# Kernel tuning notes

Measured on AMD Instinct MI355X. Metric: run time of the kernel, lower is better.

## Reference

```python
import jax, jax.numpy as jnp
import numpy as np

H = 16          # nhead
N_LAYERS = 4    # stacks (weights are SHARED across stacks, as in the torch module)
PAD_IDX = 1
EPS = 1e-6
NEG = -1e9


def _pos_encoding(S, d):
    den = jnp.exp(-jnp.arange(0, d, 2, dtype=jnp.float32) * (np.log(10000.0) / d))
    ang = jnp.arange(S, dtype=jnp.float32)[:, None] * den[None, :]  # (S, d/2)
    pe = jnp.zeros((S, d), jnp.float32)
    pe = pe.at[:, 0::2].set(jnp.sin(ang)).at[:, 1::2].set(jnp.cos(ang))
    return pe


def _layer_norm(x, g, b):
    mu = jnp.mean(x, axis=-1, keepdims=True)
    var = jnp.mean((x - mu) ** 2, axis=-1, keepdims=True)
    return (x - mu) * jax.lax.rsqrt(var + EPS) * g + b


def _split_heads(x):
    B, S, d = x.shape
    return x.reshape(B, S, H, d // H).transpose(0, 2, 1, 3)  # (B,H,S,dk)


def _mha(q_in, k_in, v_in, mask, wq, bq, wk, bk, wv, bv, wo, bo):
    q = _split_heads(q_in @ wq + bq)
    k = _split_heads(k_in @ wk + bk)
    v = _split_heads(v_in @ wv + bv)
    dk = v.shape[-1]
    score = jnp.einsum('bhqd,bhkd->bhqk', q, k) / jnp.sqrt(jnp.float32(dk))
    if mask is not None:
        score = jnp.where(mask, score, NEG)
    p = jax.nn.softmax(score, axis=-1)
    out = jnp.einsum('bhqk,bhkd->bhqd', p, v)
    B, _, S, _ = out.shape
    out = out.transpose(0, 2, 1, 3).reshape(B, S, H * dk)
    return out @ wo + bo


def setup_inputs() -> dict:
    key = jax.random.key(0)
    B, St, Sm, d, dff, V = 4, 1024, 1024, 1024, 4096, 32000
    ks = jax.random.split(key, 32)
    sc = 1.0 / np.sqrt(d)
    inp = {
        'target_result': jax.random.randint(ks[0], (B, St), 0, V),
        'memory': jax.random.normal(ks[1], (B, Sm, d), jnp.float32),
        'emb': jax.random.normal(ks[2], (V, d), jnp.float32) * sc,
        'ff_w1': jax.random.normal(ks[3], (d, dff), jnp.float32) * sc,
        'ff_b1': jnp.zeros((dff,), jnp.float32),
        'ff_w2': jax.random.normal(ks[4], (dff, d), jnp.float32) / np.sqrt(dff),
        'ff_b2': jnp.zeros((d,), jnp.float32),
        'ln_g': jnp.ones((d,), jnp.float32),
        'ln_b': jnp.zeros((d,), jnp.float32),
    }
    i = 5
    for pre in ('sa', 'xa'):
        for nm in ('q', 'k', 'v', 'o'):
            inp[f'{pre}_w{nm}'] = jax.random.normal(ks[i], (d, d), jnp.float32) * sc
            inp[f'{pre}_b{nm}'] = jnp.zeros((d,), jnp.float32)
            i += 1
    return inp


def reference(target_result, memory, emb,
              sa_wq, sa_bq, sa_wk, sa_bk, sa_wv, sa_bv, sa_wo, sa_bo,
              xa_wq, xa_bq, xa_wk, xa_bk, xa_wv, xa_bv, xa_wo, xa_bo,
              ff_w1, ff_b1, ff_w2, ff_b2, ln_g, ln_b):
    B, St = target_result.shape
    d = emb.shape[1]
    # embed + scale + positional encoding (dropout = eval/identity)
    x = emb[target_result] * jnp.sqrt(jnp.float32(d)) + _pos_encoding(St, d)[None]
    # masks: pad mask (B,1,St,1) & causal (St,St) -> (B,1,St,St); source mask all-ones -> None
    pad = (target_result != PAD_IDX)[:, None, :, None]
    causal = jnp.tril(jnp.ones((St, St), bool))[None, None]
    tgt_mask = pad & causal
    out = x
    for _ in range(N_LAYERS):
        n = _layer_norm(out, ln_g, ln_b)
        out = out + _mha(n, n, n, tgt_mask,
                         sa_wq, sa_bq, sa_wk, sa_bk, sa_wv, sa_bv, sa_wo, sa_bo)
        n = _layer_norm(out, ln_g, ln_b)
        out = out + _mha(n, memory, memory, None,
                         xa_wq, xa_bq, xa_wk, xa_bk, xa_wv, xa_bv, xa_wo, xa_bo)
        n = _layer_norm(out, ln_g, ln_b)
        out = out + (jax.nn.relu(n @ ff_w1 + ff_b1) @ ff_w2 + ff_b2)
    return _layer_norm(out, ln_g, ln_b)
```

## Files before the change

kernel.cpp:

```cpp
#include <hip/hip_runtime.h>

typedef unsigned short u16;
typedef unsigned int u32;
typedef float f32x4 __attribute__((ext_vector_type(4)));
typedef float f32x16 __attribute__((ext_vector_type(16)));
typedef __bf16 bf16x8 __attribute__((ext_vector_type(8)));
typedef short short8 __attribute__((ext_vector_type(8)));
typedef u32 u32x4 __attribute__((ext_vector_type(4)));

#define DINLINE static __device__ __forceinline__

DINLINE u16 f2bf(float f) {
  u32 u = __builtin_bit_cast(u32, f);
  u += 0x7fffu + ((u >> 16) & 1u);
  return (u16)(u >> 16);
}

DINLINE f32x4 mfma16(short8 a, short8 b, f32x4 c) {
  return __builtin_amdgcn_mfma_f32_16x16x32_bf16(
      __builtin_bit_cast(bf16x8, a), __builtin_bit_cast(bf16x8, b), c, 0, 0, 0);
}

DINLINE f32x16 mfma32(short8 a, short8 b, f32x16 c) {
  return __builtin_amdgcn_mfma_f32_32x32x16_bf16(
      __builtin_bit_cast(bf16x8, a), __builtin_bit_cast(bf16x8, b), c, 0, 0, 0);
}

DINLINE u32 cvtpk(float lo, float hi) {
  u32 r;
  asm("v_cvt_pk_bf16_f32 %0, %1, %2" : "=v"(r) : "v"(lo), "v"(hi));
  return r;
}

DINLINE void plswap(u32& a, u32& b) {
  auto r = __builtin_amdgcn_permlane32_swap(a, b, false, false);
  a = (u32)r[0];
  b = (u32)r[1];
}

DINLINE void gld16(const void* g, void* l) {
  __builtin_amdgcn_global_load_lds(
      (const __attribute__((address_space(1))) void*)g,
      (__attribute__((address_space(3))) void*)l, 16, 0, 0);
}

__global__ __launch_bounds__(256) void transpose_wt(const float* __restrict__ src,
                                                    u16* __restrict__ dst, int K, int N,
                                                    float scale) {
  __shared__ float tile[32][33];
  int n0 = blockIdx.x * 32, k0 = blockIdx.y * 32;
  int tx = threadIdx.x, ty = threadIdx.y;
#pragma unroll
  for (int j = 0; j < 32; j += 8)
    tile[ty + j][tx] = src[(size_t)(k0 + ty + j) * N + n0 + tx];
  __syncthreads();
#pragma unroll
  for (int j = 0; j < 32; j += 8)
    dst[(size_t)(n0 + ty + j) * K + k0 + tx] = f2bf(tile[tx][ty + j] * scale);
}

__global__ __launch_bounds__(256) void cvt_bf16(const float* __restrict__ src,
                                                u16* __restrict__ dst) {
  size_t i = (size_t)blockIdx.x * 256 + threadIdx.x;
  float4 v = ((const float4*)src)[i];
  u32 lo = (u32)f2bf(v.x) | ((u32)f2bf(v.y) << 16);
  u32 hi = (u32)f2bf(v.z) | ((u32)f2bf(v.w) << 16);
  uint2 o; o.x = lo; o.y = hi;
  ((uint2*)dst)[i] = o;
}

__global__ void concat3(const float* __restrict__ a, const float* __restrict__ b,
                        const float* __restrict__ c, float* __restrict__ o, float sa) {
  int i = blockIdx.x * 256 + threadIdx.x;
  float v = (i < 1024) ? a[i] * sa : (i < 2048 ? b[i - 1024] : c[i - 2048]);
  o[i] = v;
}

__global__ void scale_vec(const float* __restrict__ a, float* __restrict__ o, float s) {
  int i = blockIdx.x * 256 + threadIdx.x;
  o[i] = a[i] * s;
}

__global__ __launch_bounds__(256) void pe_k(float* __restrict__ pe) {
  int s = blockIdx.x;
  for (int c = threadIdx.x; c < 1024; c += 256) {
    int i = c >> 1;
    float den = expf(-(float)(2 * i) * 0.0089944739960705f);
    float ang = (float)s * den;
    pe[s * 1024 + c] = (c & 1) ? cosf(ang) : sinf(ang);
  }
}

__global__ __launch_bounds__(256) void embed_pe(const int* __restrict__ tgt,
                                                const float* __restrict__ emb,
                                                const float* __restrict__ pe,
                                                float* __restrict__ x) {
  int row = blockIdx.x;
  int s = row & 1023;
  int tok = tgt[row];
  float4 e = ((const float4*)(emb + (size_t)tok * 1024))[threadIdx.x];
  float4 p = ((const float4*)(pe + (size_t)s * 1024))[threadIdx.x];
  float4 o;
  o.x = e.x * 32.0f + p.x; o.y = e.y * 32.0f + p.y;
  o.z = e.z * 32.0f + p.z; o.w = e.w * 32.0f + p.w;
  ((float4*)(x + (size_t)row * 1024))[threadIdx.x] = o;
}

template <int MODE>
__global__ __launch_bounds__(256) void ln_k(const float* __restrict__ X,
                                            const float* __restrict__ g,
                                            const float* __restrict__ bta,
                                            u16* __restrict__ obf,
                                            float* __restrict__ of) {
  int row = blockIdx.x;
  int t = threadIdx.x;
  float4 v = ((const float4*)(X + (size_t)row * 1024))[t];
  float s = v.x + v.y + v.z + v.w;
  float sq = v.x * v.x + v.y * v.y + v.z * v.z + v.w * v.w;
#pragma unroll
  for (int o = 1; o < 64; o <<= 1) {
    s += __shfl_xor(s, o);
    sq += __shfl_xor(sq, o);
  }
  __shared__ float red[8];
  int wid = t >> 6;
  if ((t & 63) == 0) { red[wid * 2] = s; red[wid * 2 + 1] = sq; }
  __syncthreads();
  s = red[0] + red[2] + red[4] + red[6];
  sq = red[1] + red[3] + red[5] + red[7];
  float mean = s * (1.0f / 1024.0f);
  float var = sq * (1.0f / 1024.0f) - mean * mean;
  float rstd = rsqrtf(var + 1e-6f);
  float4 gv = ((const float4*)g)[t];
  float4 bv = ((const float4*)bta)[t];
  float y0 = (v.x - mean) * rstd * gv.x + bv.x;
  float y1 = (v.y - mean) * rstd * gv.y + bv.y;
  float y2 = (v.z - mean) * rstd * gv.z + bv.z;
  float y3 = (v.w - mean) * rstd * gv.w + bv.w;
  if (MODE == 1) {
    float4 o4; o4.x = y0; o4.y = y1; o4.z = y2; o4.w = y3;
    ((float4*)of)[(size_t)row * 256 + t] = o4;
  } else {
    u32 lo = (u32)f2bf(y0) | ((u32)f2bf(y1) << 16);
    u32 hi = (u32)f2bf(y2) | ((u32)f2bf(y3) << 16);
    uint2 o2; o2.x = lo; o2.y = hi;
    ((uint2*)obf)[(size_t)row * 256 + t] = o2;
  }
}

__global__ __launch_bounds__(256) void vtrans(const u16* __restrict__ V, int sV,
                                              u16* __restrict__ Vt) {
  __shared__ u16 tile[32][33];
  int s0 = blockIdx.x * 32, d0 = blockIdx.y * 32, bh = blockIdx.z;
  int b = bh >> 4, h = bh & 15;
  const u16* src = V + (size_t)b * 1024 * sV + h * 64;
  int tx = threadIdx.x, ty = threadIdx.y;
#pragma unroll
  for (int j = 0; j < 32; j += 8)
    tile[ty + j][tx] = src[(size_t)(s0 + ty + j) * sV + d0 + tx];
  __syncthreads();
  u16* dst = Vt + (size_t)bh * 64 * 1024;
#pragma unroll
  for (int j = 0; j < 32; j += 8)
    dst[(size_t)(d0 + ty + j) * 1024 + s0 + tx] = tile[tx][ty + j];
}

template <int BM, int EPI>
__global__ __launch_bounds__(256) void gemm2(
    const u16* __restrict__ A, const u16* __restrict__ Bt,
    const float* __restrict__ bias, float* __restrict__ X,
    u16* __restrict__ Cbf, int N, int K) {
  constexpr int ABYT = BM * 128;
  constexpr int BBYT = 128 * 128;
  constexpr int MF = BM / 32;
  __shared__ __align__(16) char smem[2 * (ABYT + BBYT)];

  const int tid = threadIdx.x;
  const int w = tid >> 6, l = tid & 63;
  const int lg = l >> 4, lc = l & 15;
  const int m0 = blockIdx.y * BM, n0 = blockIdx.x * 128;
  const int wr = w >> 1, wc = w & 1;
  const char* Ab = (const char*)A;
  const char* Bb = (const char*)Bt;
  const size_t sA = (size_t)K * 2;

  f32x4 acc[MF][4];
  const f32x4 zv = {0.f, 0.f, 0.f, 0.f};
#pragma unroll
  for (int m = 0; m < MF; ++m)
#pragma unroll
    for (int n = 0; n < 4; ++n) acc[m][n] = zv;

  const int srow = l >> 3;
  const int scol = ((l & 7) ^ srow) << 4;

  auto stage = [&](char* bufA, char* bufB, int kt) {
    const size_t kb = (size_t)kt << 7;
#pragma unroll
    for (int i = 0; i < BM / 32; ++i) {
      const int r = i * 32 + w * 8 + srow;
      gld16(Ab + (size_t)(m0 + r) * sA + kb + scol, bufA + (i * 4 + w) * 1024 + l * 16);
    }
#pragma unroll
    for (int i = 0; i < 4; ++i) {
      const int r = i * 32 + w * 8 + srow;
      gld16(Bb + (size_t)(n0 + r) * sA + kb + scol, bufB + (i * 4 + w) * 1024 + l * 16);
    }
  };

  stage(smem, smem + ABYT, 0);
  __syncthreads();

  const int nkt = K >> 6;
  int cur = 0;
  for (int kt = 0; kt < nkt; ++kt) {
    char* As = smem + cur * (ABYT + BBYT);
    char* Bs = As + ABYT;
    if (kt + 1 < nkt) {
      char* An = smem + (cur ^ 1) * (ABYT + BBYT);
      stage(An, An + ABYT, kt + 1);
    }
#pragma unroll
    for (int ks = 0; ks < 2; ++ks) {
      short8 af[MF], bf4[4];
#pragma unroll
      for (int m = 0; m < MF; ++m) {
        int row = wr * (BM / 2) + m * 16 + lc;
        int col = (ks * 64 + (lg << 4)) ^ ((row & 7) << 4);
        af[m] = *(const short8*)(As + row * 128 + col);
      }
#pragma unroll
      for (int n = 0; n < 4; ++n) {
        int row = wc * 64 + n * 16 + lc;
        int col = (ks * 64 + (lg << 4)) ^ ((row & 7) << 4);
        bf4[n] = *(const short8*)(Bs + row * 128 + col);
      }
#pragma unroll
      for (int m = 0; m < MF; ++m)
#pragma unroll
        for (int n = 0; n < 4; ++n) acc[m][n] = mfma16(af[m], bf4[n], acc[m][n]);
    }
    __syncthreads();
    cur ^= 1;
  }

  float bv[4];
#pragma unroll
  for (int n = 0; n < 4; ++n) bv[n] = bias[n0 + wc * 64 + n * 16 + lc];

  if (EPI <= 1) {
    u16* ct = (u16*)smem;
#pragma unroll
    for (int m = 0; m < MF; ++m)
#pragma unroll
      for (int n = 0; n < 4; ++n)
#pragma unroll
        for (int r = 0; r < 4; ++r) {
          int row = wr * (BM / 2) + m * 16 + (lg << 2) + r;
          int col = wc * 64 + n * 16 + lc;
          float v = acc[m][n][r] + bv[n];
          if (EPI == 1) v = v > 0.f ? v : 0.f;
          ct[row * 136 + col] = f2bf(v);
        }
    __syncthreads();
#pragma unroll
    for (int j = 0; j < BM / 16; ++j) {
      int c = j * 256 + tid;
      int row = c >> 4, colb = (c & 15) * 8;
      *(short8*)(Cbf + (size_t)(m0 + row) * N + n0 + colb) =
          *(const short8*)(ct + row * 136 + colb);
    }
  } else {
    float* cf = (float*)smem;
#pragma unroll
    for (int m = 0; m < MF; ++m)
#pragma unroll
      for (int n = 0; n < 4; ++n)
#pragma unroll
        for (int r = 0; r < 4; ++r) {
          int row = wr * (BM / 2) + m * 16 + (lg << 2) + r;
          int col = wc * 64 + n * 16 + lc;
          cf[row * 128 + col] = acc[m][n][r] + bv[n];
        }
    __syncthreads();
#pragma unroll
    for (int j = 0; j < BM / 8; ++j) {
      int c = j * 256 + tid;
      int row = c >> 5, colb = (c & 31) * 4;
      size_t idx = (size_t)(m0 + row) * N + n0 + colb;
      float4 s = *(const float4*)(cf + row * 128 + colb);
      float4 xv = *(const float4*)(X + idx);
      xv.x += s.x; xv.y += s.y; xv.z += s.z; xv.w += s.w;
      *(float4*)(X + idx) = xv;
    }
  }
}

template <bool CAUSAL>
__global__ __launch_bounds__(256) void attn_lds(
    const u16* __restrict__ Qp, int sQ, const u16* __restrict__ Kp, int sK,
    const u16* __restrict__ Vt, const int* __restrict__ tgt,
    u16* __restrict__ Out) {
  __shared__ __align__(16) char smem[2][16384];
  const int tid = threadIdx.x;
  const int w = tid >> 6, l = tid & 63;
  const int bh = blockIdx.x & 63, sub = blockIdx.x >> 6;
  const int b = bh >> 4, h = bh & 15;
  const int lq = l & 31, hi = l >> 5;
  const int qt = sub * 4 + w;
  const int q0 = qt * 32;

  const char* Kc = (const char*)(Kp + (size_t)b * 1024 * sK + h * 64);
  const char* Vc = (const char*)(Vt + (size_t)bh * 64 * 1024);
  const u16* Qh = Qp + (size_t)b * 1024 * sQ + h * 64;

  short8 qb[4];
  {
    const u16* qrow = Qh + (size_t)(q0 + lq) * sQ + hi * 8;
#pragma unroll
    for (int c = 0; c < 4; ++c) qb[c] = *(const short8*)(qrow + c * 16);
  }

  bool row_ok = true;
  int my_nkt = 16;
  int blk_nkt = CAUSAL ? (sub * 2 + 2) : 16;
  if (CAUSAL) {
    row_ok = (tgt[b * 1024 + q0 + lq] != 1);
    bool anypad_w = __any(!row_ok);
    __shared__ int s_pad;
    if (tid == 0) s_pad = 0;
    __syncthreads();
    if (anypad_w && l == 0) s_pad = 1;
    __syncthreads();
    if (s_pad) { my_nkt = 16; blk_nkt = 16; }
    else my_nkt = (qt >> 1) + 1;
  }

  const int srow = l >> 3;
  const int scol = ((l & 7) ^ srow) << 4;
  auto stage = [&](int buf, int kt) {
    const int k0 = kt * 64;
    char* Ks = smem[buf];
    char* Vs = smem[buf] + 8192;
#pragma unroll
    for (int i = 0; i < 2; ++i) {
      const int r = i * 32 + w * 8 + srow;
      gld16(Kc + (size_t)(k0 + r) * sK * 2 + scol, Ks + r * 128);
      gld16(Vc + (size_t)r * 2048 + (size_t)k0 * 2 + scol, Vs + r * 128);
    }
  };

  float m = -3.0e38f, lsum = 0.f;
  f32x16 oacc[2];
#pragma unroll
  for (int r = 0; r < 16; ++r) { oacc[0][r] = 0.f; oacc[1][r] = 0.f; }

  stage(0, 0);
  __syncthreads();
  int cur = 0;

  for (int kt = 0; kt < blk_nkt; ++kt) {
    if (kt + 1 < blk_nkt) stage(cur ^ 1, kt + 1);
    if (kt < my_nkt) {
      const char* Ks = smem[cur];
      const char* Vs = smem[cur] + 8192;
      const int k0 = kt * 64;
      f32x16 st[2];
#pragma unroll
      for (int s = 0; s < 2; ++s) {
        const int row = s * 32 + lq;
        const int swz = (row & 7) << 4;
        f32x16 a;
#pragma unroll
        for (int r = 0; r < 16; ++r) a[r] = 0.f;
#pragma unroll
        for (int c = 0; c < 4; ++c) {
          short8 kb = *(const short8*)(Ks + row * 128 + ((c * 32 + hi * 16) ^ swz));
          a = mfma32(kb, qb[c], a);
        }
        st[s] = a;
      }
      if (CAUSAL) {
#pragma unroll
        for (int s = 0; s < 2; ++s) {
          if (!row_ok || (k0 + s * 32 + 31 > q0)) {
#pragma unroll
            for (int r = 0; r < 16; ++r) {
              int kg = k0 + s * 32 + (r & 3) + 8 * (r >> 2) + 4 * hi;
              bool ok = row_ok && (kg <= q0 + lq);
              if (!ok) st[s][r] = -1e9f;
            }
          }
        }
      }
      float tm;
      {
        float v[16];
#pragma unroll
        for (int r = 0; r < 16; ++r) v[r] = fmaxf(st[0][r], st[1][r]);
#pragma unroll
        for (int w2 = 8; w2 >= 1; w2 >>= 1)
#pragma unroll
          for (int r = 0; r < w2; ++r) v[r] = fmaxf(v[r], v[r + w2]);
        tm = v[0];
      }
      tm = fmaxf(tm, __shfl_xor(tm, 32));
      if (!__all(tm <= m + 8.0f)) {
        float mn = fmaxf(m, tm);
        float alpha = __expf(m - mn);
        lsum *= alpha;
        m = mn;
#pragma unroll
        for (int r = 0; r < 16; ++r) {
          int crow = (r & 3) + 8 * (r >> 2) + 4 * hi;
          float av = __shfl(alpha, crow);
          oacc[0][r] *= av;
          oacc[1][r] *= av;
        }
      }
      float tsa0 = 0.f, tsa1 = 0.f, tsa2 = 0.f, tsa3 = 0.f;
#pragma unroll
      for (int s = 0; s < 2; ++s) {
#pragma unroll
        for (int r = 0; r < 16; ++r) {
          float e = __expf(st[s][r] - m);
          st[s][r] = e;
          if ((r & 3) == 0) tsa0 += e;
          else if ((r & 3) == 1) tsa1 += e;
          else if ((r & 3) == 2) tsa2 += e;
          else tsa3 += e;
        }
      }
      float ts = (tsa0 + tsa1) + (tsa2 + tsa3);
      ts += __shfl_xor(ts, 32);
      lsum += ts;
      short8 pa[4];
#pragma unroll
      for (int s = 0; s < 2; ++s) {
        u32 cc[8];
#pragma unroll
        for (int t = 0; t < 4; ++t) {
          cc[2 * t]     = cvtpk(st[s][4 * t + 0], st[s][4 * t + 1]);
          cc[2 * t + 1] = cvtpk(st[s][4 * t + 2], st[s][4 * t + 3]);
        }
        plswap(cc[0], cc[2]);
        plswap(cc[1], cc[3]);
        plswap(cc[4], cc[6]);
        plswap(cc[5], cc[7]);
        u32x4 w0 = {cc[0], cc[1], cc[2], cc[3]};
        u32x4 w1 = {cc[4], cc[5], cc[6], cc[7]};
        pa[2 * s]     = __builtin_bit_cast(short8, w0);
        pa[2 * s + 1] = __builtin_bit_cast(short8, w1);
      }
#pragma unroll
      for (int dt = 0; dt < 2; ++dt) {
        const int row = dt * 32 + lq;
        const int swz = (row & 7) << 4;
#pragma unroll
        for (int c = 0; c < 4; ++c) {
          short8 vb = *(const short8*)(Vs + row * 128 + ((c * 32 + hi * 16) ^ swz));
          oacc[dt] = mfma32(pa[c], vb, oacc[dt]);
        }
      }
    }
    __syncthreads();
    cur ^= 1;
  }

#pragma unroll
  for (int r = 0; r < 16; ++r) {
    int crow = (r & 3) + 8 * (r >> 2) + 4 * hi;
    float lv = __shfl(lsum, crow);
    float linv = 1.0f / lv;
    int qg = q0 + crow;
    size_t base = ((size_t)b * 1024 + qg) * 1024 + h * 64 + lq;
    Out[base] = f2bf(oacc[0][r] * linv);
    Out[base + 32] = f2bf(oacc[1][r] * linv);
  }
}

extern "C" void kernel_launch(void* const* d_in, const int* in_sizes, int n_in,
                              void* d_out, int out_size, void* d_ws, size_t ws_size,
                              hipStream_t stream) {
  const int* tgt = (const int*)d_in[0];
  const float* memory = (const float*)d_in[1];
  const float* emb = (const float*)d_in[2];
  const float* ff_w1 = (const float*)d_in[3];
  const float* ff_b1 = (const float*)d_in[4];
  const float* ff_w2 = (const float*)d_in[5];
  const float* ff_b2 = (const float*)d_in[6];
  const float* ln_g = (const float*)d_in[7];
  const float* ln_b = (const float*)d_in[8];
  const float* sa_wq = (const float*)d_in[9];
  const float* sa_bq = (const float*)d_in[10];
  const float* sa_wk = (const float*)d_in[11];
  const float* sa_bk = (const float*)d_in[12];
  const float* sa_wv = (const float*)d_in[13];
  const float* sa_bv = (const float*)d_in[14];
  const float* sa_wo = (const float*)d_in[15];
  const float* sa_bo = (const float*)d_in[16];
  const float* xa_wq = (const float*)d_in[17];
  const float* xa_bq = (const float*)d_in[18];
  const float* xa_wk = (const float*)d_in[19];
  const float* xa_bk = (const float*)d_in[20];
  const float* xa_wv = (const float*)d_in[21];
  const float* xa_bv = (const float*)d_in[22];
  const float* xa_wo = (const float*)d_in[23];
  const float* xa_bo = (const float*)d_in[24];

  char* ws = (char*)d_ws;
  size_t off = 0;
  auto alloc = [&](size_t bytes) {
    char* p = ws + off;
    off += (bytes + 255) & ~(size_t)255;
    return p;
  };
  float* x   = (float*)alloc(4096ull * 1024 * 4);
  u16* nbf   = (u16*)alloc(4096ull * 1024 * 2);
  u16* qkv   = (u16*)alloc(4096ull * 3072 * 2);
  u16* q2    = (u16*)alloc(4096ull * 1024 * 2);
  u16* attn  = (u16*)alloc(4096ull * 1024 * 2);
  u16* vt    = (u16*)alloc(64ull * 64 * 1024 * 2);
  u16* kx    = (u16*)alloc(4096ull * 1024 * 2);
  u16* vtx   = (u16*)alloc(64ull * 64 * 1024 * 2);
  u16* h1    = (u16*)alloc(4096ull * 4096 * 2);
  u16* memb  = (u16*)alloc(4096ull * 1024 * 2);
  u16* w_qkv = (u16*)alloc(3072ull * 1024 * 2);
  u16* w_sao = (u16*)alloc(1024ull * 1024 * 2);
  u16* w_xaq = (u16*)alloc(1024ull * 1024 * 2);
  u16* w_xak = (u16*)alloc(1024ull * 1024 * 2);
  u16* w_xav = (u16*)alloc(1024ull * 1024 * 2);
  u16* w_xao = (u16*)alloc(1024ull * 1024 * 2);
  u16* w_ff1 = (u16*)alloc(4096ull * 1024 * 2);
  u16* w_ff2 = (u16*)alloc(1024ull * 4096 * 2);
  float* b_qkv = (float*)alloc(3072 * 4);
  float* b_xaq = (float*)alloc(1024 * 4);
  float* pe    = (float*)alloc(1024ull * 1024 * 4);

  dim3 blk(256);
  dim3 b32(32, 8);
  const float QS = 0.125f;

  transpose_wt<<<dim3(32, 32), b32, 0, stream>>>(sa_wq, w_qkv, 1024, 1024, QS);
  transpose_wt<<<dim3(32, 32), b32, 0, stream>>>(sa_wk, w_qkv + 1024 * 1024, 1024, 1024, 1.f);
  transpose_wt<<<dim3(32, 32), b32, 0, stream>>>(sa_wv, w_qkv + 2048 * 1024, 1024, 1024, 1.f);
  transpose_wt<<<dim3(32, 32), b32, 0, stream>>>(sa_wo, w_sao, 1024, 1024, 1.f);
  transpose_wt<<<dim3(32, 32), b32, 0, stream>>>(xa_wq, w_xaq, 1024, 1024, QS);
  transpose_wt<<<dim3(32, 32), b32, 0, stream>>>(xa_wk, w_xak, 1024, 1024, 1.f);
  transpose_wt<<<dim3(32, 32), b32, 0, stream>>>(xa_wv, w_xav, 1024, 1024, 1.f);
  transpose_wt<<<dim3(32, 32), b32, 0, stream>>>(xa_wo, w_xao, 1024, 1024, 1.f);
  transpose_wt<<<dim3(128, 32), b32, 0, stream>>>(ff_w1, w_ff1, 1024, 4096, 1.f);
  transpose_wt<<<dim3(32, 128), b32, 0, stream>>>(ff_w2, w_ff2, 4096, 1024, 1.f);
  concat3<<<12, blk, 0, stream>>>(sa_bq, sa_bk, sa_bv, b_qkv, QS);
  scale_vec<<<4, blk, 0, stream>>>(xa_bq, b_xaq, QS);
  cvt_bf16<<<4096, blk, 0, stream>>>(memory, memb);
  pe_k<<<1024, blk, 0, stream>>>(pe);
  embed_pe<<<4096, blk, 0, stream>>>(tgt, emb, pe, x);

  gemm2<64, 0><<<dim3(8, 64), blk, 0, stream>>>(memb, w_xak, xa_bk, nullptr, kx, 1024, 1024);
  gemm2<64, 0><<<dim3(8, 64), blk, 0, stream>>>(memb, w_xav, xa_bv, nullptr, attn, 1024, 1024);
  vtrans<<<dim3(32, 2, 64), b32, 0, stream>>>(attn, 1024, vtx);

  for (int layer = 0; layer < 4; ++layer) {
    ln_k<0><<<4096, blk, 0, stream>>>(x, ln_g, ln_b, nbf, nullptr);
    gemm2<128, 0><<<dim3(24, 32), blk, 0, stream>>>(nbf, w_qkv, b_qkv, nullptr, qkv, 3072, 1024);
    vtrans<<<dim3(32, 2, 64), b32, 0, stream>>>(qkv + 2048, 3072, vt);
    attn_lds<true><<<512, blk, 0, stream>>>(qkv, 3072, qkv + 1024, 3072, vt, tgt, attn);
    gemm2<64, 2><<<dim3(8, 64), blk, 0, stream>>>(attn, w_sao, sa_bo, x, nullptr, 1024, 1024);
    ln_k<0><<<4096, blk, 0, stream>>>(x, ln_g, ln_b, nbf, nullptr);
    gemm2<64, 0><<<dim3(8, 64), blk, 0, stream>>>(nbf, w_xaq, b_xaq, nullptr, q2, 1024, 1024);
    attn_lds<false><<<512, blk, 0, stream>>>(q2, 1024, kx, 1024, vtx, nullptr, attn);
    gemm2<64, 2><<<dim3(8, 64), blk, 0, stream>>>(attn, w_xao, xa_bo, x, nullptr, 1024, 1024);
    ln_k<0><<<4096, blk, 0, stream>>>(x, ln_g, ln_b, nbf, nullptr);
    gemm2<128, 1><<<dim3(32, 32), blk, 0, stream>>>(nbf, w_ff1, ff_b1, nullptr, h1, 4096, 1024);
    gemm2<64, 2><<<dim3(8, 64), blk, 0, stream>>>(h1, w_ff2, ff_b2, x, nullptr, 1024, 4096);
  }
  ln_k<1><<<4096, blk, 0, stream>>>(x, ln_g, ln_b, nullptr, (float*)d_out);
}
```

Before: 1.142 ms.

## Add 256x128 triple-buffered GEMM kernel for QKV and FF1 projections

Adds a new bf16 MFMA GEMM kernel for the QKV and FF1 projections. It uses 512 threads, a 256x128 output tile and a three-stage LDS pipeline fed by direct global-to-LDS loads with XOR-swizzled rows. The epilogue applies bias (plus ReLU for FF1) and stages the bf16 tile through LDS so global stores are coalesced. The larger tile is meant to raise arithmetic intensity and hide load latency. In exchange it uses roughly 144KB of LDS, so only one block fits per CU, and fewer blocks are launched, which lowers occupancy and can leave the grid poorly balanced across CUs.

```diff
diff --git a/kernel.cpp b/kernel.cpp
--- a/kernel.cpp
+++ b/kernel.cpp
@@ -293,6 +293,126 @@
       xv.x += s.x; xv.y += s.y; xv.z += s.z; xv.w += s.w;
       *(float4*)(X + idx) = xv;
     }
+  }
+}
+
+template <int EPI>
+__global__ __launch_bounds__(512, 2) void gemm3(
+    const u16* __restrict__ A, const u16* __restrict__ Bt,
+    const float* __restrict__ bias, u16* __restrict__ Cbf, int N, int K) {
+  constexpr int ABYT = 256 * 128;
+  constexpr int BBYT = 128 * 128;
+  __shared__ __align__(16) char smem[3 * (ABYT + BBYT)];
+
+  const int tid = threadIdx.x;
+  const int w = tid >> 6, l = tid & 63;
+  const int lg = l >> 4, lc = l & 15;
+  const int m0 = blockIdx.y * 256, n0 = blockIdx.x * 128;
+  const int wr = w >> 1, wc = w & 1;
+  const char* Ab = (const char*)A;
+  const char* Bb = (const char*)Bt;
+  const size_t sA = (size_t)K * 2;
+
+  f32x4 acc[4][4];
+  const f32x4 zv = {0.f, 0.f, 0.f, 0.f};
+#pragma unroll
+  for (int m = 0; m < 4; ++m)
+#pragma unroll
+    for (int n = 0; n < 4; ++n) acc[m][n] = zv;
+
+  const int srow = l >> 3;
+  const int scol = ((l & 7) ^ srow) << 4;
+
+  auto stage = [&](char* buf, int kt) {
+    const size_t kb = (size_t)kt << 7;
+#pragma unroll
+    for (int i = 0; i < 4; ++i) {
+      const int r = i * 64 + w * 8 + srow;
+      gld16(Ab + (size_t)(m0 + r) * sA + kb + scol, buf + (i * 8 + w) * 1024 + l * 16);
+    }
+#pragma unroll
+    for (int i = 0; i < 2; ++i) {
+      const int r = i * 64 + w * 8 + srow;
+      gld16(Bb + (size_t)(n0 + r) * sA + kb + scol,
+            buf + ABYT + (i * 8 + w) * 1024 + l * 16);
+    }
+  };
+
+  auto compute = [&](const char* buf) {
+    const char* As = buf;
+    const char* Bs = buf + ABYT;
+#pragma unroll
+    for (int ks = 0; ks < 2; ++ks) {
+      short8 af[4], bf4[4];
+#pragma unroll
+      for (int m = 0; m < 4; ++m) {
+        int row = wr * 64 + m * 16 + lc;
+        int col = (ks * 64 + (lg << 4)) ^ ((row & 7) << 4);
+        af[m] = *(const short8*)(As + row * 128 + col);
+      }
+#pragma unroll
+      for (int n = 0; n < 4; ++n) {
+        int row = wc * 64 + n * 16 + lc;
+        int col = (ks * 64 + (lg << 4)) ^ ((row & 7) << 4);
+        bf4[n] = *(const short8*)(Bs + row * 128 + col);
+      }
+#pragma unroll
+      for (int m = 0; m < 4; ++m)
+#pragma unroll
+        for (int n = 0; n < 4; ++n) acc[m][n] = mfma16(af[m], bf4[n], acc[m][n]);
+    }
+  };
+
+#define GEMM3_BAR(vm)                                              \
+  __builtin_amdgcn_sched_barrier(0);                               \
+  asm volatile("s_waitcnt vmcnt(" #vm ") lgkmcnt(0)" ::: "memory"); \
+  __builtin_amdgcn_s_barrier();                                    \
+  __builtin_amdgcn_sched_barrier(0)
+
+  char* p0 = smem;
+  char* p1 = smem + (ABYT + BBYT);
+  char* p2 = smem + 2 * (ABYT + BBYT);
+
+  const int nkt = K >> 6;
+  stage(p0, 0);
+  stage(p1, 1);
+  GEMM3_BAR(6);
+
+  for (int kt = 0; kt < nkt; ++kt) {
+    if (kt + 2 < nkt) stage(p2, kt + 2);
+    compute(p0);
+    if (kt < nkt - 2) {
+      GEMM3_BAR(6);
+    } else {
+      GEMM3_BAR(0);
+    }
+    char* pr = p0; p0 = p1; p1 = p2; p2 = pr;
+  }
+#undef GEMM3_BAR
+
+  float bv[4];
+#pragma unroll
+  for (int n = 0; n < 4; ++n) bv[n] = bias[n0 + wc * 64 + n * 16 + lc];
+  u16* ct = (u16*)smem;
+#pragma unroll
+  for (int m = 0; m < 4; ++m)
+#pragma unroll
+    for (int n = 0; n < 4; ++n)
+#pragma unroll
+      for (int r = 0; r < 4; ++r) {
+        int row = wr * 64 + m * 16 + (lg << 2) + r;
+        int col = wc * 64 + n * 16 + lc;
+        float v = acc[m][n][r] + bv[n];
+        if (EPI == 1) v = v > 0.f ? v : 0.f;
+        ct[row * 136 + col] = f2bf(v);
+      }
+  __syncthreads();
+#pragma unroll
+  for (int j = 0; j < 8; ++j) {
+    int c = j * 512 + tid;
+    int row = c >> 4, colb = (c & 15) * 8;
+    *(short8*)(Cbf + (size_t)(m0 + row) * N + n0 + colb) =
+        *(const short8*)(ct + row * 136 + colb);
   }
 }
 
@@ -563,7 +683,7 @@
 
   for (int layer = 0; layer < 4; ++layer) {
     ln_k<0><<<4096, blk, 0, stream>>>(x, ln_g, ln_b, nbf, nullptr);
-    gemm2<128, 0><<<dim3(24, 32), blk, 0, stream>>>(nbf, w_qkv, b_qkv, nullptr, qkv, 3072, 1024);
+    gemm3<0><<<dim3(24, 16), dim3(512), 0, stream>>>(nbf, w_qkv, b_qkv, qkv, 3072, 1024);
     vtrans<<<dim3(32, 2, 64), b32, 0, stream>>>(qkv + 2048, 3072, vt);
     attn_lds<true><<<512, blk, 0, stream>>>(qkv, 3072, qkv + 1024, 3072, vt, tgt, attn);
     gemm2<64, 2><<<dim3(8, 64), blk, 0, stream>>>(attn, w_sao, sa_bo, x, nullptr, 1024, 1024);
@@ -572,7 +692,7 @@
     attn_lds<false><<<512, blk, 0, stream>>>(q2, 1024, kx, 1024, vtx, nullptr, attn);
     gemm2<64, 2><<<dim3(8, 64), blk, 0, stream>>>(attn, w_xao, xa_bo, x, nullptr, 1024, 1024);
     ln_k<0><<<4096, blk, 0, stream>>>(x, ln_g, ln_b, nbf, nullptr);
-    gemm2<128, 1><<<dim3(32, 32), blk, 0, stream>>>(nbf, w_ff1, ff_b1, nullptr, h1, 4096, 1024);
+    gemm3<1><<<dim3(32, 16), dim3(512), 0, stream>>>(nbf, w_ff1, ff_b1, h1, 4096, 1024);
     gemm2<64, 2><<<dim3(8, 64), blk, 0, stream>>>(h1, w_ff2, ff_b2, x, nullptr, 1024, 4096);
   }
   ln_k<1><<<4096, blk, 0, stream>>>(x, ln_g, ln_b, nullptr, (float*)d_out);
```

After: 1.191 ms. +4.3%, slower.
